# Optimization experiments

Measured on AMD Instinct MI355X. Metric: run time of the kernel, lower is better.

## Reference

```python
import jax, jax.numpy as jnp
import numpy as np

N_CELL = 50000
N_GENE = 50000
E = 800000
D = 256
EPS = 1e-5


def setup_inputs() -> dict:
    key = jax.random.key(0)
    ks = jax.random.split(key, 12)
    inp = {
        "x_cell": jax.random.normal(ks[0], (N_CELL, D), jnp.float32),
        "x_gene": jax.random.normal(ks[1], (N_GENE, D), jnp.float32),
        "W_cg": jax.random.normal(ks[2], (D, D), jnp.float32) * (1.0 / np.sqrt(D)),
        "W_gc": jax.random.normal(ks[3], (D, D), jnp.float32) * (1.0 / np.sqrt(D)),
        "W_gg": jax.random.normal(ks[4], (D, D), jnp.float32) * (1.0 / np.sqrt(D)),
        "gamma_cell": jnp.ones((D,), jnp.float32),
        "beta_cell": jnp.zeros((D,), jnp.float32),
        "gamma_gene": jnp.ones((D,), jnp.float32),
        "beta_gene": jnp.zeros((D,), jnp.float32),
        "b_cell": jnp.zeros((D,), jnp.float32),
        "b_gene": jnp.zeros((D,), jnp.float32),
        "src_cg": jax.random.randint(ks[5], (E,), 0, N_CELL, jnp.int64 if jax.config.jax_enable_x64 else jnp.int32),
        "dst_cg": jax.random.randint(ks[6], (E,), 0, N_GENE, jnp.int64 if jax.config.jax_enable_x64 else jnp.int32),
        "src_gc": jax.random.randint(ks[7], (E,), 0, N_GENE, jnp.int64 if jax.config.jax_enable_x64 else jnp.int32),
        "dst_gc": jax.random.randint(ks[8], (E,), 0, N_CELL, jnp.int64 if jax.config.jax_enable_x64 else jnp.int32),
        "src_gg": jax.random.randint(ks[9], (E,), 0, N_GENE, jnp.int64 if jax.config.jax_enable_x64 else jnp.int32),
        "dst_gg": jax.random.randint(ks[10], (E,), 0, N_GENE, jnp.int64 if jax.config.jax_enable_x64 else jnp.int32),
    }
    return inp


def _graph_conv(x_src, src, dst, n_src, n_dst, W):
    """DGL GraphConv with norm='both': D_dst^{-1/2} A D_src^{-1/2} X W."""
    ones = jnp.ones(src.shape[0], x_src.dtype)
    deg_out = jnp.clip(jax.ops.segment_sum(ones, src, num_segments=n_src), 1.0)
    deg_in = jnp.clip(jax.ops.segment_sum(ones, dst, num_segments=n_dst), 1.0)
    h = x_src * jax.lax.rsqrt(deg_out)[:, None]          # [n_src, D]
    agg = jax.ops.segment_sum(h[src], dst, num_segments=n_dst)  # gather+scatter
    agg = agg * jax.lax.rsqrt(deg_in)[:, None]           # [n_dst, D]
    return agg @ W


def _post(h, gamma, beta, b):
    # LayerNorm (affine) -> + h_bias -> relu -> dropout(p=0, eval = identity)
    mu = jnp.mean(h, axis=-1, keepdims=True)
    var = jnp.mean((h - mu) ** 2, axis=-1, keepdims=True)
    h = (h - mu) * jax.lax.rsqrt(var + EPS) * gamma + beta
    return jax.nn.relu(h + b)


def reference(x_cell, x_gene, W_cg, W_gc, W_gg, gamma_cell, beta_cell,
              gamma_gene, beta_gene, b_cell, b_gene,
              src_cg, dst_cg, src_gc, dst_gc, src_gg, dst_gg):
    # HeteroGraphConv with aggregate='sum' across relations per dst ntype
    h_gene = (_graph_conv(x_cell, src_cg, dst_cg, N_CELL, N_GENE, W_cg)
              + _graph_conv(x_gene, src_gg, dst_gg, N_GENE, N_GENE, W_gg))
    h_cell = _graph_conv(x_gene, src_gc, dst_gc, N_GENE, N_CELL, W_gc)
    out_cell = _post(h_cell, gamma_cell, beta_cell, b_cell)
    out_gene = _post(h_gene, gamma_gene, beta_gene, b_gene)
    return jnp.stack([out_cell, out_gene])  # [2, 50000, 256]
```

## Files before the change

kernel.cpp:

```cpp
#include <hip/hip_runtime.h>
#include <hip/hip_bf16.h>
#include <stdint.h>

#define DDIM 256
#define NSHARD 8
#define T1 4096
#define NCPAD 128
#define CCAP 9216

typedef short s8v __attribute__((ext_vector_type(8)));
typedef float f4v __attribute__((ext_vector_type(4)));

__device__ __forceinline__ float bf2f(unsigned u) { return __uint_as_float(u << 16); }
__device__ __forceinline__ unsigned short f2bf(float f) {
    __hip_bfloat16 h = __float2bfloat16(f);
    return *reinterpret_cast<unsigned short*>(&h);
}
__device__ __forceinline__ unsigned pack2(float a, float b) {
    return (unsigned)f2bf(a) | ((unsigned)f2bf(b) << 16);
}

__global__ void transpose3_k(const float* __restrict__ W0, const float* __restrict__ W1,
                             const float* __restrict__ W2, __hip_bfloat16* __restrict__ T0,
                             __hip_bfloat16* __restrict__ T1v, __hip_bfloat16* __restrict__ T2) {
    const float* W = (blockIdx.y == 0) ? W0 : (blockIdx.y == 1) ? W1 : W2;
    __hip_bfloat16* T = (blockIdx.y == 0) ? T0 : (blockIdx.y == 1) ? T1v : T2;
    T[blockIdx.x * DDIM + threadIdx.x] = __float2bfloat16(W[threadIdx.x * DDIM + blockIdx.x]);
}

__global__ __launch_bounds__(256) void bin1_k(
    const int* __restrict__ s0, const int* __restrict__ d0,
    const int* __restrict__ s1, const int* __restrict__ d1,
    const int* __restrict__ s2, const int* __restrict__ d2,
    int* __restrict__ cs_shard,
    int* __restrict__ gcur,
    unsigned* __restrict__ recs,
    int N, int E) {
    __shared__ unsigned stage[T1];
    __shared__ int hcnt[NCPAD], hoff[NCPAD], lbase[NCPAD], lcur[NCPAD];
    const int t = threadIdx.x;
    const int rel = blockIdx.y;
    const int* s = (rel == 0) ? s0 : (rel == 1) ? s1 : s2;
    const int* d = (rel == 0) ? d0 : (rel == 1) ? d1 : d2;
    const int e0 = blockIdx.x * T1;
    const int n = min(T1, E - e0);
    int* csb = cs_shard + ((size_t)(blockIdx.x & (NSHARD - 1)) * 3 + rel) * N;

    if (t < NCPAD) { hcnt[t] = 0; lcur[t] = 0; }
    __syncthreads();

    int ssr[T1 / 256], ddr[T1 / 256];
    #pragma unroll
    for (int k = 0; k < T1 / 256; ++k) {
        const int li = k * 256 + t;
        const bool v = li < n;
        ssr[k] = v ? s[e0 + li] : -1;
        ddr[k] = v ? d[e0 + li] : -1;
        if (v) {
            atomicAdd(&hcnt[ddr[k] >> 9], 1);
            atomicAdd(&csb[ssr[k]], 1);
        }
    }
    __syncthreads();

    if (t < 64) {
        const int a0 = hcnt[2 * t], a1 = hcnt[2 * t + 1];
        const int sum = a0 + a1;
        int incl = sum;
        #pragma unroll
        for (int off = 1; off < 64; off <<= 1) {
            const int u = __shfl_up(incl, off);
            if (t >= off) incl += u;
        }
        const int excl = incl - sum;
        hoff[2 * t] = excl;
        hoff[2 * t + 1] = excl + a0;
    }
    __syncthreads();
    if (t < NCPAD) lbase[t] = atomicAdd(&gcur[rel * NCPAD + t], hcnt[t]);
    __syncthreads();

    #pragma unroll
    for (int k = 0; k < T1 / 256; ++k) {
        if (ddr[k] >= 0) {
            const int b = ddr[k] >> 9;
            const int p = atomicAdd(&lcur[b], 1);
            stage[hoff[b] + p] = (unsigned)ssr[k] | ((unsigned)(ddr[k] & 511) << 16)
                                 | ((unsigned)b << 25);
        }
    }
    __syncthreads();

    for (int i = t; i < n; i += 256) {
        const unsigned r = stage[i];
        const int b = (int)(r >> 25);
        const int pos = lbase[b] + (i - hoff[b]);
        if (pos < CCAP)
            recs[((size_t)rel * NCPAD + b) * CCAP + pos] = r & 0x1FFFFFFu;
    }
}

__device__ __forceinline__ int deg_sum(const int* __restrict__ cs_shard, int rel, int r, int N) {
    int v = 0;
    #pragma unroll
    for (int s = 0; s < NSHARD; ++s) v += cs_shard[((size_t)s * 3 + rel) * N + r];
    return v;
}


__device__ void sort_body(int sb, unsigned char* smem,
                          const unsigned* __restrict__ recs32,
                          unsigned short* __restrict__ recs16,
                          const int* __restrict__ gcur,
                          int* __restrict__ row_beg, int* __restrict__ row_cnt,
                          int N, int ncb) {
    unsigned short* stage = (unsigned short*)smem;
    int* rc   = (int*)(smem + 18432);
    int* ro   = (int*)(smem + 20480);
    int* rcur = (int*)(smem + 22528);
    const int t = threadIdx.x;
    const int rel = sb / ncb, bin = sb % ncb;
    const size_t base = ((size_t)rel * NCPAD + bin) * CCAP;
    const int n = min(gcur[rel * NCPAD + bin], CCAP);

    for (int i = t; i < 512; i += 256) rc[i] = 0;
    __syncthreads();
    for (int i = t; i < n; i += 256)
        atomicAdd(&rc[(recs32[base + i] >> 16) & 511], 1);
    __syncthreads();
    if (t < 64) {
        int v[8], p[8], sum = 0;
        #pragma unroll
        for (int j = 0; j < 8; ++j) { v[j] = rc[t * 8 + j]; p[j] = sum; sum += v[j]; }
        int incl = sum;
        #pragma unroll
        for (int off = 1; off < 64; off <<= 1) {
            const int u = __shfl_up(incl, off);
            if (t >= off) incl += u;
        }
        const int excl = incl - sum;
        #pragma unroll
        for (int j = 0; j < 8; ++j) { ro[t * 8 + j] = excl + p[j]; rcur[t * 8 + j] = excl + p[j]; }
    }
    __syncthreads();
    for (int i = t; i < 512; i += 256) {
        const int grow = bin * 512 + i;
        if (grow < N) {
            row_cnt[(size_t)rel * N + grow] = rc[i];
            row_beg[(size_t)rel * N + grow] = (int)(base + ro[i]);
        }
    }
    for (int i = t; i < n; i += 256) {
        const unsigned r = recs32[base + i];
        const int pos = atomicAdd(&rcur[(r >> 16) & 511], 1);
        stage[pos] = (unsigned short)(r & 0xffffu);
    }
    __syncthreads();
    for (int i = t; i < n; i += 256)
        recs16[base + i] = stage[i];
}

__device__ void gemm2_body(int gb, unsigned char* smem, const float* __restrict__ X,
                           const __hip_bfloat16* __restrict__ Wt0,
                           const __hip_bfloat16* __restrict__ Wt1,
                           const int* __restrict__ cs_shard, int rel0, int rel1,
                           __hip_bfloat16* __restrict__ Y0, __hip_bfloat16* __restrict__ Y1,
                           int M, int N) {
    typedef __hip_bfloat16 (*lds_t)[2][16][DDIM];
    lds_t wlds = (lds_t)smem;
    const int t = threadIdx.x;
    const int lane = t & 63, wid = t >> 6;
    const int c = lane & 15, kb = lane >> 4;
    const int rA = gb * 128 + wid * 32 + c;
    const int rB = rA + 16;
    const bool vA = rA < M, vB = rB < M;
    const int rAc = vA ? rA : (M - 1), rBc = vB ? rB : (M - 1);

    s8v xfA[8], xfB[8];
    const float* xA = X + (size_t)rAc * DDIM;
    const float* xB = X + (size_t)rBc * DDIM;
    #pragma unroll
    for (int ks = 0; ks < 8; ++ks) {
        const int k0 = ks * 32 + kb * 8;
        const f4v a0 = *reinterpret_cast<const f4v*>(xA + k0);
        const f4v a1 = *reinterpret_cast<const f4v*>(xA + k0 + 4);
        const f4v b0 = *reinterpret_cast<const f4v*>(xB + k0);
        const f4v b1 = *reinterpret_cast<const f4v*>(xB + k0 + 4);
        union { s8v v; unsigned short u[8]; } fa, fb;
        #pragma unroll
        for (int j = 0; j < 4; ++j) {
            fa.u[j] = f2bf(a0[j]); fa.u[4 + j] = f2bf(a1[j]);
            fb.u[j] = f2bf(b0[j]); fb.u[4 + j] = f2bf(b1[j]);
        }
        xfA[ks] = fa.v; xfB[ks] = fb.v;
    }

    const int dA0 = deg_sum(cs_shard, rel0, rAc, N), dB0 = deg_sum(cs_shard, rel0, rBc, N);
    const int dA1 = deg_sum(cs_shard, rel1, rAc, N), dB1 = deg_sum(cs_shard, rel1, rBc, N);
    const float s0A = rsqrtf((float)(dA0 < 1 ? 1 : dA0));
    const float s0B = rsqrtf((float)(dB0 < 1 ? 1 : dB0));
    const float s1A = rsqrtf((float)(dA1 < 1 ? 1 : dA1));
    const float s1B = rsqrtf((float)(dB1 < 1 ? 1 : dB1));

    {
        #pragma unroll
        for (int j = 0; j < 4; ++j) {
            const int q = t + j * 256;
            const int rel = q >> 9, rt = (q >> 5) & 15, ch = q & 31;
            const __hip_bfloat16* Wsrc = rel ? Wt1 : Wt0;
            const uint4 v = *reinterpret_cast<const uint4*>(Wsrc + (size_t)rt * DDIM + ch * 8);
            *reinterpret_cast<uint4*>(&(*wlds)[0 * 2 + rel][rt][(ch ^ (rt & 7)) * 8]) = v;
        }
    }

    #pragma unroll 2
    for (int nt = 0; nt < 16; ++nt) {
        __syncthreads();
        uint4 sv[4];
        if (nt + 1 < 16) {
            #pragma unroll
            for (int j = 0; j < 4; ++j) {
                const int q = t + j * 256;
                const int rel = q >> 9, rt = (q >> 5) & 15, ch = q & 31;
                const __hip_bfloat16* Wsrc = rel ? Wt1 : Wt0;
                sv[j] = *reinterpret_cast<const uint4*>(
                    Wsrc + (size_t)((nt + 1) * 16 + rt) * DDIM + ch * 8);
            }
        }

        const int buf = nt & 1;
        f4v a00 = (f4v){0.f,0.f,0.f,0.f}, a01 = a00, a10 = a00, a11 = a00;
        #pragma unroll
        for (int ks = 0; ks < 8; ++ks) {
            const int chs = ((kb + 4 * ks) ^ (c & 7)) * 8;
            const s8v wf0 = *reinterpret_cast<const s8v*>(&(*wlds)[buf * 2 + 0][c][chs]);
            const s8v wf1 = *reinterpret_cast<const s8v*>(&(*wlds)[buf * 2 + 1][c][chs]);
            a00 = __builtin_amdgcn_mfma_f32_16x16x32_bf16(wf0, xfA[ks], a00, 0, 0, 0);
            a10 = __builtin_amdgcn_mfma_f32_16x16x32_bf16(wf0, xfB[ks], a10, 0, 0, 0);
            a01 = __builtin_amdgcn_mfma_f32_16x16x32_bf16(wf1, xfA[ks], a01, 0, 0, 0);
            a11 = __builtin_amdgcn_mfma_f32_16x16x32_bf16(wf1, xfB[ks], a11, 0, 0, 0);
        }
        const int col = nt * 16 + kb * 4;
        if (vA) {
            uint2 o0, o1;
            o0.x = pack2(a00[0] * s0A, a00[1] * s0A); o0.y = pack2(a00[2] * s0A, a00[3] * s0A);
            o1.x = pack2(a01[0] * s1A, a01[1] * s1A); o1.y = pack2(a01[2] * s1A, a01[3] * s1A);
            *reinterpret_cast<uint2*>(Y0 + (size_t)rA * DDIM + col) = o0;
            *reinterpret_cast<uint2*>(Y1 + (size_t)rA * DDIM + col) = o1;
        }
        if (vB) {
            uint2 o0, o1;
            o0.x = pack2(a10[0] * s0B, a10[1] * s0B); o0.y = pack2(a10[2] * s0B, a10[3] * s0B);
            o1.x = pack2(a11[0] * s1B, a11[1] * s1B); o1.y = pack2(a11[2] * s1B, a11[3] * s1B);
            *reinterpret_cast<uint2*>(Y0 + (size_t)rB * DDIM + col) = o0;
            *reinterpret_cast<uint2*>(Y1 + (size_t)rB * DDIM + col) = o1;
        }

        if (nt + 1 < 16) {
            #pragma unroll
            for (int j = 0; j < 4; ++j) {
                const int q = t + j * 256;
                const int rel = q >> 9, rt = (q >> 5) & 15, ch = q & 31;
                *reinterpret_cast<uint4*>(&(*wlds)[(buf ^ 1) * 2 + rel][rt][(ch ^ (rt & 7)) * 8]) = sv[j];
            }
        }
    }
}

__device__ void gemm1_body(int gb, unsigned char* smem, const float* __restrict__ X,
                           const __hip_bfloat16* __restrict__ Wt0,
                           const int* __restrict__ cs_shard, int rel0,
                           __hip_bfloat16* __restrict__ Y0, int M, int N) {
    typedef __hip_bfloat16 (*lds_t)[16][DDIM];
    lds_t wlds = (lds_t)smem;
    const int t = threadIdx.x;
    const int lane = t & 63, wid = t >> 6;
    const int c = lane & 15, kb = lane >> 4;
    const int rA = gb * 128 + wid * 32 + c;
    const int rB = rA + 16;
    const bool vA = rA < M, vB = rB < M;
    const int rAc = vA ? rA : (M - 1), rBc = vB ? rB : (M - 1);

    s8v xfA[8], xfB[8];
    const float* xA = X + (size_t)rAc * DDIM;
    const float* xB = X + (size_t)rBc * DDIM;
    #pragma unroll
    for (int ks = 0; ks < 8; ++ks) {
        const int k0 = ks * 32 + kb * 8;
        const f4v a0 = *reinterpret_cast<const f4v*>(xA + k0);
        const f4v a1 = *reinterpret_cast<const f4v*>(xA + k0 + 4);
        const f4v b0 = *reinterpret_cast<const f4v*>(xB + k0);
        const f4v b1 = *reinterpret_cast<const f4v*>(xB + k0 + 4);
        union { s8v v; unsigned short u[8]; } fa, fb;
        #pragma unroll
        for (int j = 0; j < 4; ++j) {
            fa.u[j] = f2bf(a0[j]); fa.u[4 + j] = f2bf(a1[j]);
            fb.u[j] = f2bf(b0[j]); fb.u[4 + j] = f2bf(b1[j]);
        }
        xfA[ks] = fa.v; xfB[ks] = fb.v;
    }
    const int dA0 = deg_sum(cs_shard, rel0, rAc, N), dB0 = deg_sum(cs_shard, rel0, rBc, N);
    const float s0A = rsqrtf((float)(dA0 < 1 ? 1 : dA0));
    const float s0B = rsqrtf((float)(dB0 < 1 ? 1 : dB0));

    {
        #pragma unroll
        for (int j = 0; j < 2; ++j) {
            const int q = t + j * 256;
            const int rt = (q >> 5) & 15, ch = q & 31;
            const uint4 v = *reinterpret_cast<const uint4*>(Wt0 + (size_t)rt * DDIM + ch * 8);
            *reinterpret_cast<uint4*>(&(*wlds)[0 * 16 + rt][(ch ^ (rt & 7)) * 8]) = v;
        }
    }

    #pragma unroll 2
    for (int nt = 0; nt < 16; ++nt) {
        __syncthreads();
        uint4 sv[2];
        if (nt + 1 < 16) {
            #pragma unroll
            for (int j = 0; j < 2; ++j) {
                const int q = t + j * 256;
                const int rt = (q >> 5) & 15, ch = q & 31;
                sv[j] = *reinterpret_cast<const uint4*>(
                    Wt0 + (size_t)((nt + 1) * 16 + rt) * DDIM + ch * 8);
            }
        }

        const int buf = nt & 1;
        f4v a00 = (f4v){0.f,0.f,0.f,0.f}, a10 = a00;
        #pragma unroll
        for (int ks = 0; ks < 8; ++ks) {
            const int chs = ((kb + 4 * ks) ^ (c & 7)) * 8;
            const s8v wf0 = *reinterpret_cast<const s8v*>(&(*wlds)[buf * 16 + c][chs]);
            a00 = __builtin_amdgcn_mfma_f32_16x16x32_bf16(wf0, xfA[ks], a00, 0, 0, 0);
            a10 = __builtin_amdgcn_mfma_f32_16x16x32_bf16(wf0, xfB[ks], a10, 0, 0, 0);
        }
        const int col = nt * 16 + kb * 4;
        if (vA) {
            uint2 o;
            o.x = pack2(a00[0] * s0A, a00[1] * s0A); o.y = pack2(a00[2] * s0A, a00[3] * s0A);
            *reinterpret_cast<uint2*>(Y0 + (size_t)rA * DDIM + col) = o;
        }
        if (vB) {
            uint2 o;
            o.x = pack2(a10[0] * s0B, a10[1] * s0B); o.y = pack2(a10[2] * s0B, a10[3] * s0B);
            *reinterpret_cast<uint2*>(Y0 + (size_t)rB * DDIM + col) = o;
        }

        if (nt + 1 < 16) {
            #pragma unroll
            for (int j = 0; j < 2; ++j) {
                const int q = t + j * 256;
                const int rt = (q >> 5) & 15, ch = q & 31;
                *reinterpret_cast<uint4*>(&(*wlds)[(buf ^ 1) * 16 + rt][(ch ^ (rt & 7)) * 8]) = sv[j];
            }
        }
    }
}

__global__ __launch_bounds__(256, 4) void mid_k(
    const unsigned* __restrict__ recs32, unsigned short* __restrict__ recs16,
    const int* __restrict__ gcur,
    int* __restrict__ row_beg, int* __restrict__ row_cnt,
    const float* __restrict__ x_gene, const float* __restrict__ x_cell,
    const __hip_bfloat16* __restrict__ Wt_gc, const __hip_bfloat16* __restrict__ Wt_gg,
    const __hip_bfloat16* __restrict__ Wt_cg,
    const int* __restrict__ cs_shard,
    __hip_bfloat16* __restrict__ Y_gc, __hip_bfloat16* __restrict__ Y_gg,
    __hip_bfloat16* __restrict__ Y_cg,
    int N, int ncb, int gemmBlocks) {
    __shared__ uint4 smem4[2048];
    unsigned char* smem = (unsigned char*)smem4;
    const int bid = blockIdx.x;
    if (bid < gemmBlocks) {
        gemm2_body(bid, smem, x_gene, Wt_gc, Wt_gg, cs_shard, 0, 2, Y_gc, Y_gg, N, N);
    } else if (bid < 2 * gemmBlocks) {
        gemm1_body(bid - gemmBlocks, smem, x_cell, Wt_cg, cs_shard, 1, Y_cg, N, N);
    } else {
        sort_body(bid - 2 * gemmBlocks, smem, recs32, recs16, gcur,
                  row_beg, row_cnt, N, ncb);
    }
}

__device__ __forceinline__ void addv(f4v& a, uint2 v) {
    a[0] += bf2f(v.x & 0xffffu);
    a[1] += bf2f(v.x >> 16);
    a[2] += bf2f(v.y & 0xffffu);
    a[3] += bf2f(v.y >> 16);
}

__device__ __forceinline__ f4v segsum(const unsigned short* __restrict__ recs, int beg, int n,
                                      const __hip_bfloat16* __restrict__ Y, int lane) {
    f4v a = (f4v){0.f, 0.f, 0.f, 0.f};
    for (int j0 = 0; j0 < n; j0 += 64) {
        const int chunk = min(64, n - j0);
        unsigned rv = 0;
        if (lane < chunk) rv = recs[beg + j0 + lane];
        int t = 0;
        for (; t + 8 <= chunk; t += 8) {
            uint2 v[8];
            #pragma unroll
            for (int i = 0; i < 8; ++i) {
                const int s = (int)__shfl(rv, t + i);
                v[i] = reinterpret_cast<const uint2*>(Y + (size_t)s * DDIM)[lane];
            }
            #pragma unroll
            for (int i = 0; i < 8; ++i) addv(a, v[i]);
        }
        if (t + 4 <= chunk) {
            uint2 v[4];
            #pragma unroll
            for (int i = 0; i < 4; ++i) {
                const int s = (int)__shfl(rv, t + i);
                v[i] = reinterpret_cast<const uint2*>(Y + (size_t)s * DDIM)[lane];
            }
            #pragma unroll
            for (int i = 0; i < 4; ++i) addv(a, v[i]);
            t += 4;
        }
        for (; t < chunk; ++t) {
            const int s = (int)__shfl(rv, t);
            addv(a, reinterpret_cast<const uint2*>(Y + (size_t)s * DDIM)[lane]);
        }
    }
    return a;
}

__global__ __launch_bounds__(256, 4) void gather_ln_k(
    const unsigned short* __restrict__ recs,
    const int* __restrict__ beg0, const int* __restrict__ cnt0,
    const __hip_bfloat16* __restrict__ Y0,
    const int* __restrict__ beg1, const int* __restrict__ cnt1,
    const __hip_bfloat16* __restrict__ Y1,
    const float* __restrict__ gamma, const float* __restrict__ beta,
    const float* __restrict__ bias, float* __restrict__ out, int n_dst) {
    const int lane = threadIdx.x & 63, wid = threadIdx.x >> 6;
    const int row = blockIdx.x * 4 + wid;
    if (row >= n_dst) return;

    const int n0 = cnt0[row];
    f4v a = segsum(recs, beg0[row], n0, Y0, lane);
    a *= rsqrtf((float)(n0 < 1 ? 1 : n0));
    if (beg1 != nullptr) {
        const int n1 = cnt1[row];
        f4v a1 = segsum(recs, beg1[row], n1, Y1, lane);
        a += a1 * rsqrtf((float)(n1 < 1 ? 1 : n1));
    }

    float s1 = a[0] + a[1] + a[2] + a[3];
    float s2 = a[0]*a[0] + a[1]*a[1] + a[2]*a[2] + a[3]*a[3];
    #pragma unroll
    for (int off = 1; off < 64; off <<= 1) {
        s1 += __shfl_xor(s1, off);
        s2 += __shfl_xor(s2, off);
    }
    const float mu = s1 * (1.f / 256.f);
    float var = s2 * (1.f / 256.f) - mu * mu;
    var = fmaxf(var, 0.f);
    const float rs = rsqrtf(var + 1e-5f);

    const f4v g  = reinterpret_cast<const f4v*>(gamma)[lane];
    const f4v be = reinterpret_cast<const f4v*>(beta)[lane];
    const f4v bb = reinterpret_cast<const f4v*>(bias)[lane];
    f4v o;
    #pragma unroll
    for (int j = 0; j < 4; ++j) {
        float v = (a[j] - mu) * rs * g[j] + be[j] + bb[j];
        o[j] = fmaxf(v, 0.f);
    }
    reinterpret_cast<f4v*>(out + (size_t)row * DDIM)[lane] = o;
}

extern "C" void kernel_launch(void* const* d_in, const int* in_sizes, int n_in,
                              void* d_out, int out_size, void* d_ws, size_t ws_size,
                              hipStream_t stream) {
    const float* x_cell     = (const float*)d_in[0];
    const float* x_gene     = (const float*)d_in[1];
    const float* W_cg       = (const float*)d_in[2];
    const float* W_gc       = (const float*)d_in[3];
    const float* W_gg       = (const float*)d_in[4];
    const float* gamma_cell = (const float*)d_in[5];
    const float* beta_cell  = (const float*)d_in[6];
    const float* gamma_gene = (const float*)d_in[7];
    const float* beta_gene  = (const float*)d_in[8];
    const float* b_cell     = (const float*)d_in[9];
    const float* b_gene     = (const float*)d_in[10];
    const int* src_cg = (const int*)d_in[11];
    const int* dst_cg = (const int*)d_in[12];
    const int* src_gc = (const int*)d_in[13];
    const int* dst_gc = (const int*)d_in[14];
    const int* src_gg = (const int*)d_in[15];
    const int* dst_gg = (const int*)d_in[16];

    const int N = in_sizes[0] / DDIM;
    const int E = in_sizes[11];
    const int ncb = (N + 511) >> 9;

    char* wsb = (char*)d_ws;
    size_t off = 0;
    __hip_bfloat16* Y_gc = (__hip_bfloat16*)(wsb + off); off += (size_t)N * DDIM * 2;
    unsigned* recs32 = (unsigned*)(wsb + off);           off += (size_t)3 * NCPAD * CCAP * 4;
    unsigned short* recs16 = (unsigned short*)(wsb + off); off += (size_t)3 * NCPAD * CCAP * 2;
    int* row_beg = (int*)(wsb + off);                    off += (size_t)3 * N * 4;
    int* row_cnt = (int*)(wsb + off);                    off += (size_t)3 * N * 4;
    const size_t zeroOff = off;
    int* cs_shard = (int*)(wsb + off);                   off += (size_t)NSHARD * 3 * N * 4;
    int* gcur     = (int*)(wsb + off);                   off += (size_t)3 * NCPAD * 4;
    const size_t zeroBytes = off - zeroOff;
    __hip_bfloat16* Wt_gc = (__hip_bfloat16*)(wsb + off); off += (size_t)DDIM * DDIM * 2;
    __hip_bfloat16* Wt_cg = (__hip_bfloat16*)(wsb + off); off += (size_t)DDIM * DDIM * 2;
    __hip_bfloat16* Wt_gg = (__hip_bfloat16*)(wsb + off);

    int* beg_gc = row_beg, *beg_cg = row_beg + N, *beg_gg = row_beg + 2 * N;
    int* cnt_gc = row_cnt, *cnt_cg = row_cnt + N, *cnt_gg = row_cnt + 2 * N;

    float* out_cell = (float*)d_out;
    float* out_gene = out_cell + (size_t)N * DDIM;
    __hip_bfloat16* Y_cg = (__hip_bfloat16*)d_out;
    __hip_bfloat16* Y_gg = Y_cg + (size_t)N * DDIM;

    const int binBlocks  = (E + T1 - 1) / T1;
    const int gemmBlocks = (N + 127) / 128;
    const int gatherBlocks = (N + 3) / 4;

    transpose3_k<<<dim3(DDIM, 3), DDIM, 0, stream>>>(W_gc, W_cg, W_gg, Wt_gc, Wt_cg, Wt_gg);
    hipMemsetAsync(wsb + zeroOff, 0, zeroBytes, stream);

    bin1_k<<<dim3(binBlocks, 3), 256, 0, stream>>>(src_gc, dst_gc, src_cg, dst_cg,
                                                   src_gg, dst_gg, cs_shard, gcur, recs32, N, E);

    mid_k<<<2 * gemmBlocks + 3 * ncb, 256, 0, stream>>>(
        recs32, recs16, gcur, row_beg, row_cnt, x_gene, x_cell,
        Wt_gc, Wt_gg, Wt_cg, cs_shard, Y_gc, Y_gg, Y_cg, N, ncb, gemmBlocks);

    gather_ln_k<<<gatherBlocks, 256, 0, stream>>>(recs16, beg_cg, cnt_cg, Y_cg,
                                                  beg_gg, cnt_gg, Y_gg,
                                                  gamma_gene, beta_gene, b_gene, out_gene, N);
    gather_ln_k<<<gatherBlocks, 256, 0, stream>>>(recs16, beg_gc, cnt_gc, Y_gc,
                                                  nullptr, nullptr, nullptr,
                                                  gamma_cell, beta_cell, b_cell, out_cell, N);
}
```

Before: 395.6 us.

## Split degree counting out and co-schedule edge binning with GEMMs

Source-degree counting moves into a small standalone count kernel, so the edge-binning work can run as extra blocks inside the combined GEMM kernel instead of as a separate launch before it. The per-bin sort moves into its own kernel that runs after the binning and GEMMs finish. The goal is to overlap the memory-bound binning with the dense GEMM work and keep the dependency chain short. In exchange there is one more launch, the source indices are read a second time, and the bin blocks now share LDS and occupancy limits with the GEMM blocks.

```diff
diff --git a/kernel.cpp b/kernel.cpp
--- a/kernel.cpp
+++ b/kernel.cpp
@@ -28,23 +28,43 @@
     T[blockIdx.x * DDIM + threadIdx.x] = __float2bfloat16(W[threadIdx.x * DDIM + blockIdx.x]);
 }
 
-__global__ __launch_bounds__(256) void bin1_k(
-    const int* __restrict__ s0, const int* __restrict__ d0,
-    const int* __restrict__ s1, const int* __restrict__ d1,
-    const int* __restrict__ s2, const int* __restrict__ d2,
-    int* __restrict__ cs_shard,
-    int* __restrict__ gcur,
-    unsigned* __restrict__ recs,
-    int N, int E) {
-    __shared__ unsigned stage[T1];
-    __shared__ int hcnt[NCPAD], hoff[NCPAD], lbase[NCPAD], lcur[NCPAD];
+__global__ void count_k(const int* __restrict__ s0, const int* __restrict__ s1,
+                        const int* __restrict__ s2, int* __restrict__ cs_shard,
+                        int N, int E) {
+    const int i = blockIdx.x * blockDim.x + threadIdx.x;
+    if (i >= E) return;
+    const int sh = blockIdx.x & (NSHARD - 1);
+    int* csb = cs_shard + (size_t)sh * 3 * N;
+    atomicAdd(csb + s0[i], 1);
+    atomicAdd(csb + N + s1[i], 1);
+    atomicAdd(csb + 2 * N + s2[i], 1);
+}
+
+__device__ __forceinline__ int deg_sum(const int* __restrict__ cs_shard, int rel, int r, int N) {
+    int v = 0;
+    #pragma unroll
+    for (int s = 0; s < NSHARD; ++s) v += cs_shard[((size_t)s * 3 + rel) * N + r];
+    return v;
+}
+
+
+__device__ void bin1_body(int idx, unsigned char* smem,
+                          const int* __restrict__ s0, const int* __restrict__ d0,
+                          const int* __restrict__ s1, const int* __restrict__ d1,
+                          const int* __restrict__ s2, const int* __restrict__ d2,
+                          int* __restrict__ gcur, unsigned* __restrict__ recs,
+                          int N, int E, int binBlocks) {
+    unsigned* stage = (unsigned*)smem;
+    int* hcnt  = (int*)(smem + 16384);
+    int* hoff  = (int*)(smem + 16896);
+    int* lbase = (int*)(smem + 17408);
+    int* lcur  = (int*)(smem + 17920);
     const int t = threadIdx.x;
-    const int rel = blockIdx.y;
+    const int rel = idx / binBlocks, eb = idx % binBlocks;
     const int* s = (rel == 0) ? s0 : (rel == 1) ? s1 : s2;
     const int* d = (rel == 0) ? d0 : (rel == 1) ? d1 : d2;
-    const int e0 = blockIdx.x * T1;
+    const int e0 = eb * T1;
     const int n = min(T1, E - e0);
-    int* csb = cs_shard + ((size_t)(blockIdx.x & (NSHARD - 1)) * 3 + rel) * N;
 
     if (t < NCPAD) { hcnt[t] = 0; lcur[t] = 0; }
     __syncthreads();
@@ -56,10 +76,7 @@
         const bool v = li < n;
         ssr[k] = v ? s[e0 + li] : -1;
         ddr[k] = v ? d[e0 + li] : -1;
-        if (v) {
-            atomicAdd(&hcnt[ddr[k] >> 9], 1);
-            atomicAdd(&csb[ssr[k]], 1);
-        }
+        if (v) atomicAdd(&hcnt[ddr[k] >> 9], 1);
     }
     __syncthreads();
 
@@ -98,66 +115,6 @@
         if (pos < CCAP)
             recs[((size_t)rel * NCPAD + b) * CCAP + pos] = r & 0x1FFFFFFu;
     }
-}
-
-__device__ __forceinline__ int deg_sum(const int* __restrict__ cs_shard, int rel, int r, int N) {
-    int v = 0;
-    #pragma unroll
-    for (int s = 0; s < NSHARD; ++s) v += cs_shard[((size_t)s * 3 + rel) * N + r];
-    return v;
-}
-
-
-__device__ void sort_body(int sb, unsigned char* smem,
-                          const unsigned* __restrict__ recs32,
-                          unsigned short* __restrict__ recs16,
-                          const int* __restrict__ gcur,
-                          int* __restrict__ row_beg, int* __restrict__ row_cnt,
-                          int N, int ncb) {
-    unsigned short* stage = (unsigned short*)smem;
-    int* rc   = (int*)(smem + 18432);
-    int* ro   = (int*)(smem + 20480);
-    int* rcur = (int*)(smem + 22528);
-    const int t = threadIdx.x;
-    const int rel = sb / ncb, bin = sb % ncb;
-    const size_t base = ((size_t)rel * NCPAD + bin) * CCAP;
-    const int n = min(gcur[rel * NCPAD + bin], CCAP);
-
-    for (int i = t; i < 512; i += 256) rc[i] = 0;
-    __syncthreads();
-    for (int i = t; i < n; i += 256)
-        atomicAdd(&rc[(recs32[base + i] >> 16) & 511], 1);
-    __syncthreads();
-    if (t < 64) {
-        int v[8], p[8], sum = 0;
-        #pragma unroll
-        for (int j = 0; j < 8; ++j) { v[j] = rc[t * 8 + j]; p[j] = sum; sum += v[j]; }
-        int incl = sum;
-        #pragma unroll
-        for (int off = 1; off < 64; off <<= 1) {
-            const int u = __shfl_up(incl, off);
-            if (t >= off) incl += u;
-        }
-        const int excl = incl - sum;
-        #pragma unroll
-        for (int j = 0; j < 8; ++j) { ro[t * 8 + j] = excl + p[j]; rcur[t * 8 + j] = excl + p[j]; }
-    }
-    __syncthreads();
-    for (int i = t; i < 512; i += 256) {
-        const int grow = bin * 512 + i;
-        if (grow < N) {
-            row_cnt[(size_t)rel * N + grow] = rc[i];
-            row_beg[(size_t)rel * N + grow] = (int)(base + ro[i]);
-        }
-    }
-    for (int i = t; i < n; i += 256) {
-        const unsigned r = recs32[base + i];
-        const int pos = atomicAdd(&rcur[(r >> 16) & 511], 1);
-        stage[pos] = (unsigned short)(r & 0xffffu);
-    }
-    __syncthreads();
-    for (int i = t; i < n; i += 256)
-        recs16[base + i] = stage[i];
 }
 
 __device__ void gemm2_body(int gb, unsigned char* smem, const float* __restrict__ X,
@@ -359,17 +316,18 @@
     }
 }
 
-__global__ __launch_bounds__(256, 4) void mid_k(
-    const unsigned* __restrict__ recs32, unsigned short* __restrict__ recs16,
-    const int* __restrict__ gcur,
-    int* __restrict__ row_beg, int* __restrict__ row_cnt,
+__global__ __launch_bounds__(256, 4) void mega_k(
+    const int* __restrict__ s0, const int* __restrict__ d0,
+    const int* __restrict__ s1, const int* __restrict__ d1,
+    const int* __restrict__ s2, const int* __restrict__ d2,
+    int* __restrict__ gcur, unsigned* __restrict__ recs32,
     const float* __restrict__ x_gene, const float* __restrict__ x_cell,
     const __hip_bfloat16* __restrict__ Wt_gc, const __hip_bfloat16* __restrict__ Wt_gg,
     const __hip_bfloat16* __restrict__ Wt_cg,
     const int* __restrict__ cs_shard,
     __hip_bfloat16* __restrict__ Y_gc, __hip_bfloat16* __restrict__ Y_gg,
     __hip_bfloat16* __restrict__ Y_cg,
-    int N, int ncb, int gemmBlocks) {
+    int N, int E, int binBlocks, int gemmBlocks) {
     __shared__ uint4 smem4[2048];
     unsigned char* smem = (unsigned char*)smem4;
     const int bid = blockIdx.x;
@@ -378,9 +336,57 @@
     } else if (bid < 2 * gemmBlocks) {
         gemm1_body(bid - gemmBlocks, smem, x_cell, Wt_cg, cs_shard, 1, Y_cg, N, N);
     } else {
-        sort_body(bid - 2 * gemmBlocks, smem, recs32, recs16, gcur,
-                  row_beg, row_cnt, N, ncb);
-    }
+        bin1_body(bid - 2 * gemmBlocks, smem, s0, d0, s1, d1, s2, d2,
+                  gcur, recs32, N, E, binBlocks);
+    }
+}
+
+__global__ __launch_bounds__(256) void sort_k(
+    const unsigned* __restrict__ recs32, unsigned short* __restrict__ recs16,
+    const int* __restrict__ gcur,
+    int* __restrict__ row_beg, int* __restrict__ row_cnt, int N, int ncb) {
+    __shared__ unsigned short stage[CCAP];
+    __shared__ int rc[512], ro[512], rcur[512];
+    const int t = threadIdx.x;
+    const int rel = blockIdx.x / ncb, bin = blockIdx.x % ncb;
+    const size_t base = ((size_t)rel * NCPAD + bin) * CCAP;
+    const int n = min(gcur[rel * NCPAD + bin], CCAP);
+
+    for (int i = t; i < 512; i += 256) rc[i] = 0;
+    __syncthreads();
+    for (int i = t; i < n; i += 256)
+        atomicAdd(&rc[(recs32[base + i] >> 16) & 511], 1);
+    __syncthreads();
+    if (t < 64) {
+        int v[8], p[8], sum = 0;
+        #pragma unroll
+        for (int j = 0; j < 8; ++j) { v[j] = rc[t * 8 + j]; p[j] = sum; sum += v[j]; }
+        int incl = sum;
+        #pragma unroll
+        for (int off = 1; off < 64; off <<= 1) {
+            const int u = __shfl_up(incl, off);
+            if (t >= off) incl += u;
+        }
+        const int excl = incl - sum;
+        #pragma unroll
+        for (int j = 0; j < 8; ++j) { ro[t * 8 + j] = excl + p[j]; rcur[t * 8 + j] = excl + p[j]; }
+    }
+    __syncthreads();
+    for (int i = t; i < 512; i += 256) {
+        const int grow = bin * 512 + i;
+        if (grow < N) {
+            row_cnt[(size_t)rel * N + grow] = rc[i];
+            row_beg[(size_t)rel * N + grow] = (int)(base + ro[i]);
+        }
+    }
+    for (int i = t; i < n; i += 256) {
+        const unsigned r = recs32[base + i];
+        const int pos = atomicAdd(&rcur[(r >> 16) & 511], 1);
+        stage[pos] = (unsigned short)(r & 0xffffu);
+    }
+    __syncthreads();
+    for (int i = t; i < n; i += 256)
+        recs16[base + i] = stage[i];
 }
 
 __device__ __forceinline__ void addv(f4v& a, uint2 v) {
@@ -520,19 +526,22 @@
     __hip_bfloat16* Y_cg = (__hip_bfloat16*)d_out;
     __hip_bfloat16* Y_gg = Y_cg + (size_t)N * DDIM;
 
-    const int binBlocks  = (E + T1 - 1) / T1;
-    const int gemmBlocks = (N + 127) / 128;
+    const int binBlocks   = (E + T1 - 1) / T1;
+    const int gemmBlocks  = (N + 127) / 128;
     const int gatherBlocks = (N + 3) / 4;
+    const int countBlocks = (E + 255) / 256;
 
     transpose3_k<<<dim3(DDIM, 3), DDIM, 0, stream>>>(W_gc, W_cg, W_gg, Wt_gc, Wt_cg, Wt_gg);
     hipMemsetAsync(wsb + zeroOff, 0, zeroBytes, stream);
 
-    bin1_k<<<dim3(binBlocks, 3), 256, 0, stream>>>(src_gc, dst_gc, src_cg, dst_cg,
-                                                   src_gg, dst_gg, cs_shard, gcur, recs32, N, E);
-
-    mid_k<<<2 * gemmBlocks + 3 * ncb, 256, 0, stream>>>(
-        recs32, recs16, gcur, row_beg, row_cnt, x_gene, x_cell,
-        Wt_gc, Wt_gg, Wt_cg, cs_shard, Y_gc, Y_gg, Y_cg, N, ncb, gemmBlocks);
+    count_k<<<countBlocks, 256, 0, stream>>>(src_gc, src_cg, src_gg, cs_shard, N, E);
+
+    mega_k<<<2 * gemmBlocks + 3 * binBlocks, 256, 0, stream>>>(
+        src_gc, dst_gc, src_cg, dst_cg, src_gg, dst_gg,
+        gcur, recs32, x_gene, x_cell, Wt_gc, Wt_gg, Wt_cg, cs_shard,
+        Y_gc, Y_gg, Y_cg, N, E, binBlocks, gemmBlocks);
+
+    sort_k<<<3 * ncb, 256, 0, stream>>>(recs32, recs16, gcur, row_beg, row_cnt, N, ncb);
 
     gather_ln_k<<<gatherBlocks, 256, 0, stream>>>(recs16, beg_cg, cnt_cg, Y_cg,
                                                   beg_gg, cnt_gg, Y_gg,
```

Result: slower. 410.3 us (+3.7%).
